# Optimization experiments

Hardware: AMD Instinct MI355X
Metric: run time of the kernel (lower is better)

The kernel has to match this reference:

```python
import jax, jax.numpy as jnp
import numpy as np

EMBED_DIM = 768
NUM_HEADS = 12
D_K = EMBED_DIM // NUM_HEADS


def setup_inputs() -> dict:
    key = jax.random.key(0)
    ks = jax.random.split(key, 9)
    b, s, d = 4, 2048, EMBED_DIM
    scale = 1.0 / np.sqrt(d)
    x = jax.random.normal(ks[0], (b, s, d), dtype=jnp.float32)
    return {
        "x": x,
        "w_q": jax.random.normal(ks[1], (d, d), dtype=jnp.float32) * scale,
        "b_q": jnp.zeros((d,), dtype=jnp.float32),
        "w_k": jax.random.normal(ks[2], (d, d), dtype=jnp.float32) * scale,
        "b_k": jnp.zeros((d,), dtype=jnp.float32),
        "w_v": jax.random.normal(ks[3], (d, d), dtype=jnp.float32) * scale,
        "b_v": jnp.zeros((d,), dtype=jnp.float32),
        "w_o": jax.random.normal(ks[4], (d, d), dtype=jnp.float32) * scale,
        "b_o": jnp.zeros((d,), dtype=jnp.float32),
    }


def reference(x, w_q, b_q, w_k, b_k, w_v, b_v, w_o, b_o):
    b, s, d = x.shape
    h, dk = NUM_HEADS, D_K
    # projections (torch Linear: x @ W^T + b)
    q = (x @ w_q.T + b_q).reshape(b, s, h, dk).transpose(0, 2, 1, 3)
    k = (x @ w_k.T + b_k).reshape(b, s, h, dk).transpose(0, 2, 1, 3)
    v = (x @ w_v.T + b_v).reshape(b, s, h, dk).transpose(0, 2, 1, 3)
    # causal attention: full [b,h,s,s] scores as in the original
    scores = jnp.einsum("bhqd,bhkd->bhqk", q, k) / jnp.sqrt(jnp.float32(dk))
    causal = jnp.tril(jnp.ones((s, s), dtype=bool))
    scores = jnp.where(causal[None, None], scores, -jnp.inf)
    attn = jax.nn.softmax(scores, axis=-1)
    out = jnp.einsum("bhqk,bhkd->bhqd", attn, v)
    out = out.transpose(0, 2, 1, 3).reshape(b, s, h * dk)
    return out @ w_o.T + b_o
```

## Files before the change

kernel.cpp:

```cpp
#include <hip/hip_runtime.h>
#include <hip/hip_bf16.h>
#include <stdint.h>

typedef short bf16x8 __attribute__((ext_vector_type(8)));
typedef float f32x4 __attribute__((ext_vector_type(4)));
typedef unsigned short u16;


__device__ __forceinline__ u16 f2bf_bits(float f) {
    __hip_bfloat16 h = __float2bfloat16(f);
    return __builtin_bit_cast(u16, h);
}

__device__ __forceinline__ uint32_t pack2bf(float a, float b) {
    uint32_t ua = __builtin_bit_cast(uint32_t, a) + 0x8000u;
    uint32_t ub = __builtin_bit_cast(uint32_t, b) + 0x8000u;
    return __builtin_amdgcn_perm(ub, ua, 0x07060302u);
}

__device__ __forceinline__ void gld_lds16(const void* g, void* l) {
    __builtin_amdgcn_global_load_lds(
        (const __attribute__((address_space(1))) void*)g,
        (__attribute__((address_space(3))) void*)l, 16, 0, 0);
}

#define CEXP 0.18033688011112042f


__global__ __launch_bounds__(256) void cast_all_kernel(
    const float* __restrict__ x, const float* __restrict__ w0,
    const float* __restrict__ w1, const float* __restrict__ w2,
    const float* __restrict__ w3, u16* __restrict__ xb,
    u16* __restrict__ o0, u16* __restrict__ o1,
    u16* __restrict__ o2, u16* __restrict__ o3,
    const float* __restrict__ bq, const float* __restrict__ bk,
    const float* __restrict__ bv, float* __restrict__ biasf) {
    int gid = blockIdx.x * 256 + threadIdx.x;
    const float* s;
    u16* d;
    int off;
    if (gid < 1572864) {
        s = x; d = xb; off = gid;
    } else {
        int g2 = gid - 1572864;
        int which = g2 / 147456;
        off = g2 - which * 147456;
        s = which == 0 ? w0 : which == 1 ? w1 : which == 2 ? w2 : w3;
        d = which == 0 ? o0 : which == 1 ? o1 : which == 2 ? o2 : o3;
    }
    float4 v = ((const float4*)s)[off];
    ushort4 u;
    u.x = f2bf_bits(v.x); u.y = f2bf_bits(v.y);
    u.z = f2bf_bits(v.z); u.w = f2bf_bits(v.w);
    ((ushort4*)d)[off] = u;
    if (gid < 2304) {
        float bb = gid < 768 ? bq[gid] : gid < 1536 ? bk[gid - 768] : bv[gid - 1536];
        biasf[gid] = bb;
    }
}


template <int RT, int MODE>
__global__ __launch_bounds__(256) void gemm_xwt(
    const u16* __restrict__ X, const u16* __restrict__ W,
    const float* __restrict__ bias, float* __restrict__ Cf,
    u16* __restrict__ Cb, u16* __restrict__ Vt, int K, int NC) {
    constexpr int JR = RT / 32;
    __shared__ u16 lsX[RT * 64];
    __shared__ u16 lsW[128 * 64];
    const int tid = threadIdx.x;
    const int w = tid >> 6, lane = tid & 63;
    const int quad = lane >> 4, l15 = lane & 15;
    const int m0 = blockIdx.y * RT, n0 = blockIdx.x * 128;
    const int wr = (w >> 1) * (RT / 2), wc = (w & 1) * 64;
    const int rr = lane >> 3, c8 = lane & 7;

    f32x4 acc[JR][4];
    for (int j = 0; j < JR; ++j)
        for (int i = 0; i < 4; ++i) acc[j][i] = (f32x4){0.f, 0.f, 0.f, 0.f};

    const int KT = K / 64;
    for (int kt = 0; kt < KT; ++kt) {
        const int k0 = kt * 64;
        __syncthreads();
        for (int cb = w; cb < RT / 8; cb += 4) {
            int row = cb * 8 + rr;
            int cg = c8 ^ ((rr ^ cb) & 7);
            gld_lds16(X + (size_t)(m0 + row) * K + k0 + cg * 8, &lsX[cb * 512]);
        }
        for (int cb = w; cb < 16; cb += 4) {
            int row = cb * 8 + rr;
            int cg = c8 ^ ((rr ^ cb) & 7);
            gld_lds16(W + (size_t)(n0 + row) * K + k0 + cg * 8, &lsW[cb * 512]);
        }
        __syncthreads();

        for (int kk = 0; kk < 2; ++kk) {
            bf16x8 xf[JR], wf[4];
            for (int j = 0; j < JR; ++j) {
                int row = wr + j * 16 + l15;
                int slot = (kk * 4 + quad) ^ ((row ^ (row >> 3)) & 7);
                xf[j] = *(const bf16x8*)&lsX[row * 64 + slot * 8];
            }
            for (int i = 0; i < 4; ++i) {
                int row = wc + i * 16 + l15;
                int slot = (kk * 4 + quad) ^ ((row ^ (row >> 3)) & 7);
                wf[i] = *(const bf16x8*)&lsW[row * 64 + slot * 8];
            }
            for (int j = 0; j < JR; ++j)
                for (int i = 0; i < 4; ++i)
                    acc[j][i] = __builtin_amdgcn_mfma_f32_16x16x32_bf16(
                        wf[i], xf[j], acc[j][i], 0, 0, 0);
        }
    }

    const bool vtile = (MODE == 2) && (n0 >= 1536);
    for (int i = 0; i < 4; ++i) {
        int c0 = n0 + wc + i * 16 + quad * 4;
        float4 bv4 = *(const float4*)&bias[c0];
        for (int j = 0; j < JR; ++j) {
            int row = m0 + wr + j * 16 + l15;
            float v0 = acc[j][i][0] + bv4.x;
            float v1 = acc[j][i][1] + bv4.y;
            float v2 = acc[j][i][2] + bv4.z;
            float v3 = acc[j][i][3] + bv4.w;
            if (MODE == 1) {
                float4 o4 = {v0, v1, v2, v3};
                *(float4*)&Cf[(size_t)row * NC + c0] = o4;
            } else if (vtile) {
                int d = c0 - 1536;
                int bq_ = row >> 11;
                int s = row & 2047;
                int h = d >> 6, dd = d & 63;
                size_t base = ((size_t)(bq_ * 12 + h) * 64 + dd) * 2048 + s;
                Vt[base]          = f2bf_bits(v0);
                Vt[base + 2048]   = f2bf_bits(v1);
                Vt[base + 4096]   = f2bf_bits(v2);
                Vt[base + 6144]   = f2bf_bits(v3);
            } else {
                uint2 pk = {pack2bf(v0, v1), pack2bf(v2, v3)};
                *(uint2*)&Cb[(size_t)row * NC + c0] = pk;
            }
        }
    }
}


__global__ __launch_bounds__(256, 3) void attn_kernel(
    const u16* __restrict__ QKV, const u16* __restrict__ Vt, u16* __restrict__ O) {
    __shared__ u16 lsQ[128 * 64];
    __shared__ u16 lsK[64 * 64];
    __shared__ u16 lsV[64 * 64];
    __shared__ u16 lsP[4][32 * 72];

    int bx = blockIdx.x;
    int bh = bx % 48;
    int qtb = 15 - (bx / 48);
    int b = bh / 12, h = bh % 12;
    int tid = threadIdx.x, w = tid >> 6, lane = tid & 63;
    int quad = lane >> 4, l15 = lane & 15;
    int rr = lane >> 3, c8 = lane & 7;

    for (int cb = w; cb < 16; cb += 4) {
        int row = cb * 8 + rr;
        int cg = c8 ^ ((rr ^ cb) & 7);
        gld_lds16(QKV + (size_t)(b * 2048 + qtb * 128 + row) * 2304 + h * 64 + cg * 8,
                  &lsQ[cb * 512]);
    }
    __syncthreads();

    bf16x8 q0[2], q1[2];
    for (int g = 0; g < 2; ++g) {
        int rowq = g * 64 + w * 16 + l15;
        int swq = (rowq ^ (rowq >> 3)) & 7;
        q0[g] = *(const bf16x8*)&lsQ[rowq * 64 + ((0 + quad) ^ swq) * 8];
        q1[g] = *(const bf16x8*)&lsQ[rowq * 64 + ((4 + quad) ^ swq) * 8];
    }

    f32x4 oacc0[4], oacc1[4];
    for (int dt = 0; dt < 4; ++dt) {
        oacc0[dt] = (f32x4){0.f, 0.f, 0.f, 0.f};
        oacc1[dt] = (f32x4){0.f, 0.f, 0.f, 0.f};
    }
    float li0 = 0.f, li1 = 0.f;
    u16* Pw = lsP[w];
    const int qrel = w * 16 + l15;
    const int ktmax = 2 * qtb + 1;

    for (int kt = 0; kt <= ktmax; ++kt) {
        __syncthreads();
        for (int cb = w; cb < 8; cb += 4) {
            int row = cb * 8 + rr;
            int cg = c8 ^ ((rr ^ cb) & 7);
            gld_lds16(QKV + (size_t)(b * 2048 + kt * 64 + row) * 2304 + 768 + h * 64 + cg * 8,
                      &lsK[cb * 512]);
            gld_lds16(Vt + (size_t)(bh * 64 + row) * 2048 + kt * 64 + cg * 8,
                      &lsV[cb * 512]);
        }
        __syncthreads();

        const bool do0 = (kt <= 2 * qtb);

        f32x4 S0[4], S1[4];
        for (int ct = 0; ct < 4; ++ct) {
            int rowk = ct * 16 + l15;
            int swk = (rowk ^ (rowk >> 3)) & 7;
            bf16x8 k0 = *(const bf16x8*)&lsK[rowk * 64 + ((0 + quad) ^ swk) * 8];
            bf16x8 k1 = *(const bf16x8*)&lsK[rowk * 64 + ((4 + quad) ^ swk) * 8];
            f32x4 z = (f32x4){0.f, 0.f, 0.f, 0.f};
            S1[ct] = __builtin_amdgcn_mfma_f32_16x16x32_bf16(k0, q0[1], z, 0, 0, 0);
            S1[ct] = __builtin_amdgcn_mfma_f32_16x16x32_bf16(k1, q1[1], S1[ct], 0, 0, 0);
            if (do0) {
                S0[ct] = __builtin_amdgcn_mfma_f32_16x16x32_bf16(k0, q0[0], z, 0, 0, 0);
                S0[ct] = __builtin_amdgcn_mfma_f32_16x16x32_bf16(k1, q1[0], S0[ct], 0, 0, 0);
            }
        }

        if (kt == 2 * qtb) {
            for (int ct = 0; ct < 4; ++ct) {
                int kbase = ct * 16 + quad * 4;
                for (int r = 0; r < 4; ++r)
                    if (kbase + r > qrel) S0[ct][r] = -1e30f;
            }
        }
        if (kt == 2 * qtb + 1) {
            for (int ct = 0; ct < 4; ++ct) {
                int kbase = ct * 16 + quad * 4;
                for (int r = 0; r < 4; ++r)
                    if (kbase + r > qrel) S1[ct][r] = -1e30f;
            }
        }

        if (do0) {
            u16* Pr = &Pw[(size_t)l15 * 72];
            for (int ct = 0; ct < 4; ++ct) {
                float p0 = __builtin_amdgcn_exp2f(S0[ct][0] * CEXP);
                float p1 = __builtin_amdgcn_exp2f(S0[ct][1] * CEXP);
                float p2 = __builtin_amdgcn_exp2f(S0[ct][2] * CEXP);
                float p3 = __builtin_amdgcn_exp2f(S0[ct][3] * CEXP);
                li0 += (p0 + p1) + (p2 + p3);
                uint2 pk = {pack2bf(p0, p1), pack2bf(p2, p3)};
                *(uint2*)&Pr[ct * 16 + quad * 4] = pk;
            }
        }
        {
            u16* Pr = &Pw[(size_t)(16 + l15) * 72];
            for (int ct = 0; ct < 4; ++ct) {
                float p0 = __builtin_amdgcn_exp2f(S1[ct][0] * CEXP);
                float p1 = __builtin_amdgcn_exp2f(S1[ct][1] * CEXP);
                float p2 = __builtin_amdgcn_exp2f(S1[ct][2] * CEXP);
                float p3 = __builtin_amdgcn_exp2f(S1[ct][3] * CEXP);
                li1 += (p0 + p1) + (p2 + p3);
                uint2 pk = {pack2bf(p0, p1), pack2bf(p2, p3)};
                *(uint2*)&Pr[ct * 16 + quad * 4] = pk;
            }
        }

        for (int ks = 0; ks < 2; ++ks) {
            bf16x8 bp1 = *(const bf16x8*)&Pw[(size_t)(16 + l15) * 72 + ks * 32 + quad * 8];
            bf16x8 bp0;
            if (do0) bp0 = *(const bf16x8*)&Pw[(size_t)l15 * 72 + ks * 32 + quad * 8];
            for (int dt = 0; dt < 4; ++dt) {
                int rowv = dt * 16 + l15;
                int swv = (rowv ^ (rowv >> 3)) & 7;
                bf16x8 av = *(const bf16x8*)&lsV[rowv * 64 + ((ks * 4 + quad) ^ swv) * 8];
                oacc1[dt] = __builtin_amdgcn_mfma_f32_16x16x32_bf16(av, bp1, oacc1[dt], 0, 0, 0);
                if (do0)
                    oacc0[dt] = __builtin_amdgcn_mfma_f32_16x16x32_bf16(av, bp0, oacc0[dt], 0, 0, 0);
            }
        }
    }

    li0 += __shfl_xor(li0, 16, 64);
    li0 += __shfl_xor(li0, 32, 64);
    li1 += __shfl_xor(li1, 16, 64);
    li1 += __shfl_xor(li1, 32, 64);
    float inv0 = 1.0f / li0, inv1 = 1.0f / li1;

    for (int g = 0; g < 2; ++g) {
        float inv = g ? inv1 : inv0;
        f32x4* oa = g ? oacc1 : oacc0;
        int row = qtb * 128 + g * 64 + w * 16 + l15;
        for (int dt = 0; dt < 4; ++dt) {
            uint2 pk = {pack2bf(oa[dt][0] * inv, oa[dt][1] * inv),
                        pack2bf(oa[dt][2] * inv, oa[dt][3] * inv)};
            *(uint2*)&O[(size_t)(b * 2048 + row) * 768 + h * 64 + dt * 16 + quad * 4] = pk;
        }
    }
}


extern "C" void kernel_launch(void* const* d_in, const int* in_sizes, int n_in,
                              void* d_out, int out_size, void* d_ws, size_t ws_size,
                              hipStream_t stream) {
    const float* x  = (const float*)d_in[0];
    const float* wq = (const float*)d_in[1];
    const float* bq = (const float*)d_in[2];
    const float* wk = (const float*)d_in[3];
    const float* bk = (const float*)d_in[4];
    const float* wv = (const float*)d_in[5];
    const float* bv = (const float*)d_in[6];
    const float* wo = (const float*)d_in[7];
    const float* bo = (const float*)d_in[8];
    float* out = (float*)d_out;

    char* ws = (char*)d_ws;
    u16*   xb    = (u16*)(ws + 0);
    u16*   Wf    = (u16*)(ws + 12582912);
    u16*   wob   = (u16*)(ws + 16121856);
    float* biasf = (float*)(ws + 17301504);
    u16*   QKVb  = (u16*)(ws + 17310720);
    u16*   Vtw   = (u16*)(ws + 55059456);
    u16*   Ow    = (u16*)(ws + 67642368);

    cast_all_kernel<<<8448, 256, 0, stream>>>(x, wq, wk, wv, wo,
                                              xb, Wf, Wf + 589824, Wf + 1179648, wob,
                                              bq, bk, bv, biasf);

    gemm_xwt<128, 2><<<dim3(18, 64), 256, 0, stream>>>(xb, Wf, biasf, nullptr, QKVb,
                                                       Vtw, 768, 2304);
    attn_kernel<<<768, 256, 0, stream>>>(QKVb, Vtw, Ow);
    gemm_xwt<64, 1><<<dim3(6, 128), 256, 0, stream>>>(Ow, wob, bo, out, nullptr,
                                                      nullptr, 768, 768);
}
```

Measured before the change: 215.3 us.

## Double-buffer GEMM and attention loads, fold softmax scale into Wq, MFMA row sums

The GEMM and attention kernels now double-buffer their LDS tiles, prefetching the next K tile while the current one is computed, so each iteration needs one barrier instead of two. The softmax exponent scale is folded into W_q and b_q during the cast, removing a multiply per score. Row sums are computed with an MFMA against a ones vector, replacing per-lane adds and cross-lane shuffles. The V-transpose epilogue is staged through LDS so it can use coalesced 16-byte stores, and launch-bound occupancy hints are added. The extra LDS may reduce occupancy, and summing the bf16-rounded probabilities slightly changes numerics.

```diff
diff --git a/kernel.cpp b/kernel.cpp
--- a/kernel.cpp
+++ b/kernel.cpp
@@ -39,6 +39,7 @@
     const float* s;
     u16* d;
     int off;
+    float mul = 1.0f;
     if (gid < 1572864) {
         s = x; d = xb; off = gid;
     } else {
@@ -47,27 +48,30 @@
         off = g2 - which * 147456;
         s = which == 0 ? w0 : which == 1 ? w1 : which == 2 ? w2 : w3;
         d = which == 0 ? o0 : which == 1 ? o1 : which == 2 ? o2 : o3;
+        if (which == 0) mul = CEXP;
     }
     float4 v = ((const float4*)s)[off];
     ushort4 u;
-    u.x = f2bf_bits(v.x); u.y = f2bf_bits(v.y);
-    u.z = f2bf_bits(v.z); u.w = f2bf_bits(v.w);
+    u.x = f2bf_bits(v.x * mul); u.y = f2bf_bits(v.y * mul);
+    u.z = f2bf_bits(v.z * mul); u.w = f2bf_bits(v.w * mul);
     ((ushort4*)d)[off] = u;
     if (gid < 2304) {
-        float bb = gid < 768 ? bq[gid] : gid < 1536 ? bk[gid - 768] : bv[gid - 1536];
+        float bb = gid < 768 ? bq[gid] * CEXP
+                             : gid < 1536 ? bk[gid - 768] : bv[gid - 1536];
         biasf[gid] = bb;
     }
 }
 
 
-template <int RT, int MODE>
-__global__ __launch_bounds__(256) void gemm_xwt(
+template <int RT, int MODE, int MINW>
+__global__ __launch_bounds__(256, MINW) void gemm_xwt(
     const u16* __restrict__ X, const u16* __restrict__ W,
     const float* __restrict__ bias, float* __restrict__ Cf,
     u16* __restrict__ Cb, u16* __restrict__ Vt, int K, int NC) {
     constexpr int JR = RT / 32;
-    __shared__ u16 lsX[RT * 64];
-    __shared__ u16 lsW[128 * 64];
+    constexpr int XSZ = RT * 64;
+    constexpr int WSZ = 128 * 64;
+    __shared__ u16 pool[2 * XSZ + 2 * WSZ];
     const int tid = threadIdx.x;
     const int w = tid >> 6, lane = tid & 63;
     const int quad = lane >> 4, l15 = lane & 15;
@@ -75,71 +79,97 @@
     const int wr = (w >> 1) * (RT / 2), wc = (w & 1) * 64;
     const int rr = lane >> 3, c8 = lane & 7;
 
+    auto stage = [&](int kt, int pb) {
+        const int k0 = kt * 64;
+        u16* bx = pool + pb * XSZ;
+        u16* bw = pool + 2 * XSZ + pb * WSZ;
+        for (int cb = w; cb < RT / 8; cb += 4) {
+            int row = cb * 8 + rr;
+            int cg = c8 ^ ((rr ^ cb) & 7);
+            gld_lds16(X + (size_t)(m0 + row) * K + k0 + cg * 8, &bx[cb * 512]);
+        }
+        for (int cb = w; cb < 16; cb += 4) {
+            int row = cb * 8 + rr;
+            int cg = c8 ^ ((rr ^ cb) & 7);
+            gld_lds16(W + (size_t)(n0 + row) * K + k0 + cg * 8, &bw[cb * 512]);
+        }
+    };
+
     f32x4 acc[JR][4];
     for (int j = 0; j < JR; ++j)
         for (int i = 0; i < 4; ++i) acc[j][i] = (f32x4){0.f, 0.f, 0.f, 0.f};
 
     const int KT = K / 64;
+    stage(0, 0);
+    __syncthreads();
     for (int kt = 0; kt < KT; ++kt) {
-        const int k0 = kt * 64;
-        __syncthreads();
-        for (int cb = w; cb < RT / 8; cb += 4) {
-            int row = cb * 8 + rr;
-            int cg = c8 ^ ((rr ^ cb) & 7);
-            gld_lds16(X + (size_t)(m0 + row) * K + k0 + cg * 8, &lsX[cb * 512]);
-        }
-        for (int cb = w; cb < 16; cb += 4) {
-            int row = cb * 8 + rr;
-            int cg = c8 ^ ((rr ^ cb) & 7);
-            gld_lds16(W + (size_t)(n0 + row) * K + k0 + cg * 8, &lsW[cb * 512]);
-        }
-        __syncthreads();
-
+        const int pb = kt & 1;
+        if (kt + 1 < KT) stage(kt + 1, pb ^ 1);
+        const u16* bx = pool + pb * XSZ;
+        const u16* bw = pool + 2 * XSZ + pb * WSZ;
         for (int kk = 0; kk < 2; ++kk) {
             bf16x8 xf[JR], wf[4];
             for (int j = 0; j < JR; ++j) {
                 int row = wr + j * 16 + l15;
                 int slot = (kk * 4 + quad) ^ ((row ^ (row >> 3)) & 7);
-                xf[j] = *(const bf16x8*)&lsX[row * 64 + slot * 8];
+                xf[j] = *(const bf16x8*)&bx[row * 64 + slot * 8];
             }
             for (int i = 0; i < 4; ++i) {
                 int row = wc + i * 16 + l15;
                 int slot = (kk * 4 + quad) ^ ((row ^ (row >> 3)) & 7);
-                wf[i] = *(const bf16x8*)&lsW[row * 64 + slot * 8];
+                wf[i] = *(const bf16x8*)&bw[row * 64 + slot * 8];
             }
             for (int j = 0; j < JR; ++j)
                 for (int i = 0; i < 4; ++i)
                     acc[j][i] = __builtin_amdgcn_mfma_f32_16x16x32_bf16(
                         wf[i], xf[j], acc[j][i], 0, 0, 0);
         }
+        __syncthreads();
     }
 
     const bool vtile = (MODE == 2) && (n0 >= 1536);
-    for (int i = 0; i < 4; ++i) {
-        int c0 = n0 + wc + i * 16 + quad * 4;
-        float4 bv4 = *(const float4*)&bias[c0];
-        for (int j = 0; j < JR; ++j) {
-            int row = m0 + wr + j * 16 + l15;
-            float v0 = acc[j][i][0] + bv4.x;
-            float v1 = acc[j][i][1] + bv4.y;
-            float v2 = acc[j][i][2] + bv4.z;
-            float v3 = acc[j][i][3] + bv4.w;
-            if (MODE == 1) {
-                float4 o4 = {v0, v1, v2, v3};
-                *(float4*)&Cf[(size_t)row * NC + c0] = o4;
-            } else if (vtile) {
-                int d = c0 - 1536;
-                int bq_ = row >> 11;
-                int s = row & 2047;
-                int h = d >> 6, dd = d & 63;
-                size_t base = ((size_t)(bq_ * 12 + h) * 64 + dd) * 2048 + s;
-                Vt[base]          = f2bf_bits(v0);
-                Vt[base + 2048]   = f2bf_bits(v1);
-                Vt[base + 4096]   = f2bf_bits(v2);
-                Vt[base + 6144]   = f2bf_bits(v3);
-            } else {
-                uint2 pk = {pack2bf(v0, v1), pack2bf(v2, v3)};
-                *(uint2*)&Cb[(size_t)row * NC + c0] = pk;
+    if (vtile) {
+        u16* T2 = pool;
+        for (int i = 0; i < 4; ++i) {
+            int nl = wc + i * 16 + quad * 4;
+            int c0 = n0 + nl;
+            float4 bv4 = *(const float4*)&bias[c0];
+            for (int j = 0; j < JR; ++j) {
+                int ml = wr + j * 16 + l15;
+                T2[(nl + 0) * 136 + ml] = f2bf_bits(acc[j][i][0] + bv4.x);
+                T2[(nl + 1) * 136 + ml] = f2bf_bits(acc[j][i][1] + bv4.y);
+                T2[(nl + 2) * 136 + ml] = f2bf_bits(acc[j][i][2] + bv4.z);
+                T2[(nl + 3) * 136 + ml] = f2bf_bits(acc[j][i][3] + bv4.w);
+            }
+        }
+        __syncthreads();
+        int sc = (tid & 15) * 8;
+        int bq_ = m0 >> 11;
+        int s0 = m0 & 2047;
+        for (int rnd = 0; rnd < 8; ++rnd) {
+            int dl = (tid >> 4) + rnd * 16;
+            bf16x8 vv = *(const bf16x8*)&T2[dl * 136 + sc];
+            int dg = n0 + dl - 1536;
+            int h = dg >> 6, dd = dg & 63;
+            *(bf16x8*)&Vt[((size_t)(bq_ * 12 + h) * 64 + dd) * 2048 + s0 + sc] = vv;
+        }
+    } else {
+        for (int i = 0; i < 4; ++i) {
+            int c0 = n0 + wc + i * 16 + quad * 4;
+            float4 bv4 = *(const float4*)&bias[c0];
+            for (int j = 0; j < JR; ++j) {
+                int row = m0 + wr + j * 16 + l15;
+                float v0 = acc[j][i][0] + bv4.x;
+                float v1 = acc[j][i][1] + bv4.y;
+                float v2 = acc[j][i][2] + bv4.z;
+                float v3 = acc[j][i][3] + bv4.w;
+                if (MODE == 1) {
+                    float4 o4 = {v0, v1, v2, v3};
+                    *(float4*)&Cf[(size_t)row * NC + c0] = o4;
+                } else {
+                    uint2 pk = {pack2bf(v0, v1), pack2bf(v2, v3)};
+                    *(uint2*)&Cb[(size_t)row * NC + c0] = pk;
+                }
             }
         }
     }
@@ -148,9 +178,7 @@
 
 __global__ __launch_bounds__(256, 3) void attn_kernel(
     const u16* __restrict__ QKV, const u16* __restrict__ Vt, u16* __restrict__ O) {
-    __shared__ u16 lsQ[128 * 64];
-    __shared__ u16 lsK[64 * 64];
-    __shared__ u16 lsV[64 * 64];
+    __shared__ u16 lsKV[2 * 128 * 64];
     __shared__ u16 lsP[4][32 * 72];
 
     int bx = blockIdx.x;
@@ -161,52 +189,66 @@
     int quad = lane >> 4, l15 = lane & 15;
     int rr = lane >> 3, c8 = lane & 7;
 
-    for (int cb = w; cb < 16; cb += 4) {
-        int row = cb * 8 + rr;
-        int cg = c8 ^ ((rr ^ cb) & 7);
-        gld_lds16(QKV + (size_t)(b * 2048 + qtb * 128 + row) * 2304 + h * 64 + cg * 8,
-                  &lsQ[cb * 512]);
-    }
+    auto stageKV = [&](int kt, int pb) {
+        u16* dst = lsKV + pb * 8192;
+        for (int cb = w; cb < 16; cb += 4) {
+            int r = (cb & 7) * 8 + rr;
+            int cg = c8 ^ ((rr ^ cb) & 7);
+            const u16* g = (cb < 8)
+                ? QKV + (size_t)(b * 2048 + kt * 64 + r) * 2304 + 768 + h * 64 + cg * 8
+                : Vt + (size_t)(bh * 64 + r) * 2048 + kt * 64 + cg * 8;
+            gld_lds16(g, &dst[cb * 512]);
+        }
+    };
+
+    {
+        u16* qs = lsKV + 8192;
+        for (int cb = w; cb < 16; cb += 4) {
+            int row = cb * 8 + rr;
+            int cg = c8 ^ ((rr ^ cb) & 7);
+            gld_lds16(QKV + (size_t)(b * 2048 + qtb * 128 + row) * 2304 + h * 64 + cg * 8,
+                      &qs[cb * 512]);
+        }
+    }
+    stageKV(0, 0);
     __syncthreads();
 
     bf16x8 q0[2], q1[2];
     for (int g = 0; g < 2; ++g) {
+        const u16* qs = lsKV + 8192;
         int rowq = g * 64 + w * 16 + l15;
         int swq = (rowq ^ (rowq >> 3)) & 7;
-        q0[g] = *(const bf16x8*)&lsQ[rowq * 64 + ((0 + quad) ^ swq) * 8];
-        q1[g] = *(const bf16x8*)&lsQ[rowq * 64 + ((4 + quad) ^ swq) * 8];
-    }
-
-    f32x4 oacc0[4], oacc1[4];
+        q0[g] = *(const bf16x8*)&qs[rowq * 64 + ((0 + quad) ^ swq) * 8];
+        q1[g] = *(const bf16x8*)&qs[rowq * 64 + ((4 + quad) ^ swq) * 8];
+    }
+    __syncthreads();
+
+    const bf16x8 ones = {(short)0x3F80, (short)0x3F80, (short)0x3F80, (short)0x3F80,
+                         (short)0x3F80, (short)0x3F80, (short)0x3F80, (short)0x3F80};
+    f32x4 oacc0[4], oacc1[4], lacc0, lacc1;
     for (int dt = 0; dt < 4; ++dt) {
         oacc0[dt] = (f32x4){0.f, 0.f, 0.f, 0.f};
         oacc1[dt] = (f32x4){0.f, 0.f, 0.f, 0.f};
     }
-    float li0 = 0.f, li1 = 0.f;
+    lacc0 = (f32x4){0.f, 0.f, 0.f, 0.f};
+    lacc1 = (f32x4){0.f, 0.f, 0.f, 0.f};
     u16* Pw = lsP[w];
     const int qrel = w * 16 + l15;
     const int ktmax = 2 * qtb + 1;
 
     for (int kt = 0; kt <= ktmax; ++kt) {
-        __syncthreads();
-        for (int cb = w; cb < 8; cb += 4) {
-            int row = cb * 8 + rr;
-            int cg = c8 ^ ((rr ^ cb) & 7);
-            gld_lds16(QKV + (size_t)(b * 2048 + kt * 64 + row) * 2304 + 768 + h * 64 + cg * 8,
-                      &lsK[cb * 512]);
-            gld_lds16(Vt + (size_t)(bh * 64 + row) * 2048 + kt * 64 + cg * 8,
-                      &lsV[cb * 512]);
-        }
-        __syncthreads();
-
+        const int pb = kt & 1;
+        if (kt < ktmax) stageKV(kt + 1, pb ^ 1);
+        const u16* Kf = lsKV + pb * 8192;
+        const u16* Vf = Kf + 4096;
         const bool do0 = (kt <= 2 * qtb);
 
         f32x4 S0[4], S1[4];
         for (int ct = 0; ct < 4; ++ct) {
             int rowk = ct * 16 + l15;
             int swk = (rowk ^ (rowk >> 3)) & 7;
-            bf16x8 k0 = *(const bf16x8*)&lsK[rowk * 64 + ((0 + quad) ^ swk) * 8];
-            bf16x8 k1 = *(const bf16x8*)&lsK[rowk * 64 + ((4 + quad) ^ swk) * 8];
+            bf16x8 k0 = *(const bf16x8*)&Kf[rowk * 64 + ((0 + quad) ^ swk) * 8];
+            bf16x8 k1 = *(const bf16x8*)&Kf[rowk * 64 + ((4 + quad) ^ swk) * 8];
             f32x4 z = (f32x4){0.f, 0.f, 0.f, 0.f};
             S1[ct] = __builtin_amdgcn_mfma_f32_16x16x32_bf16(k0, q0[1], z, 0, 0, 0);
             S1[ct] = __builtin_amdgcn_mfma_f32_16x16x32_bf16(k1, q1[1], S1[ct], 0, 0, 0);
@@ -234,11 +276,10 @@
         if (do0) {
             u16* Pr = &Pw[(size_t)l15 * 72];
             for (int ct = 0; ct < 4; ++ct) {
-                float p0 = __builtin_amdgcn_exp2f(S0[ct][0] * CEXP);
-                float p1 = __builtin_amdgcn_exp2f(S0[ct][1] * CEXP);
-                float p2 = __builtin_amdgcn_exp2f(S0[ct][2] * CEXP);
-                float p3 = __builtin_amdgcn_exp2f(S0[ct][3] * CEXP);
-                li0 += (p0 + p1) + (p2 + p3);
+                float p0 = __builtin_amdgcn_exp2f(S0[ct][0]);
+                float p1 = __builtin_amdgcn_exp2f(S0[ct][1]);
+                float p2 = __builtin_amdgcn_exp2f(S0[ct][2]);
+                float p3 = __builtin_amdgcn_exp2f(S0[ct][3]);
                 uint2 pk = {pack2bf(p0, p1), pack2bf(p2, p3)};
                 *(uint2*)&Pr[ct * 16 + quad * 4] = pk;
             }
@@ -246,11 +287,10 @@
         {
             u16* Pr = &Pw[(size_t)(16 + l15) * 72];
             for (int ct = 0; ct < 4; ++ct) {
-                float p0 = __builtin_amdgcn_exp2f(S1[ct][0] * CEXP);
-                float p1 = __builtin_amdgcn_exp2f(S1[ct][1] * CEXP);
-                float p2 = __builtin_amdgcn_exp2f(S1[ct][2] * CEXP);
-                float p3 = __builtin_amdgcn_exp2f(S1[ct][3] * CEXP);
-                li1 += (p0 + p1) + (p2 + p3);
+                float p0 = __builtin_amdgcn_exp2f(S1[ct][0]);
+                float p1 = __builtin_amdgcn_exp2f(S1[ct][1]);
+                float p2 = __builtin_amdgcn_exp2f(S1[ct][2]);
+                float p3 = __builtin_amdgcn_exp2f(S1[ct][3]);
                 uint2 pk = {pack2bf(p0, p1), pack2bf(p2, p3)};
                 *(uint2*)&Pr[ct * 16 + quad * 4] = pk;
             }
@@ -260,23 +300,22 @@
             bf16x8 bp1 = *(const bf16x8*)&Pw[(size_t)(16 + l15) * 72 + ks * 32 + quad * 8];
             bf16x8 bp0;
             if (do0) bp0 = *(const bf16x8*)&Pw[(size_t)l15 * 72 + ks * 32 + quad * 8];
+            lacc1 = __builtin_amdgcn_mfma_f32_16x16x32_bf16(ones, bp1, lacc1, 0, 0, 0);
+            if (do0)
+                lacc0 = __builtin_amdgcn_mfma_f32_16x16x32_bf16(ones, bp0, lacc0, 0, 0, 0);
             for (int dt = 0; dt < 4; ++dt) {
                 int rowv = dt * 16 + l15;
                 int swv = (rowv ^ (rowv >> 3)) & 7;
-                bf16x8 av = *(const bf16x8*)&lsV[rowv * 64 + ((ks * 4 + quad) ^ swv) * 8];
+                bf16x8 av = *(const bf16x8*)&Vf[rowv * 64 + ((ks * 4 + quad) ^ swv) * 8];
                 oacc1[dt] = __builtin_amdgcn_mfma_f32_16x16x32_bf16(av, bp1, oacc1[dt], 0, 0, 0);
                 if (do0)
                     oacc0[dt] = __builtin_amdgcn_mfma_f32_16x16x32_bf16(av, bp0, oacc0[dt], 0, 0, 0);
             }
         }
-    }
-
-    li0 += __shfl_xor(li0, 16, 64);
-    li0 += __shfl_xor(li0, 32, 64);
-    li1 += __shfl_xor(li1, 16, 64);
-    li1 += __shfl_xor(li1, 32, 64);
-    float inv0 = 1.0f / li0, inv1 = 1.0f / li1;
-
+        __syncthreads();
+    }
+
+    float inv0 = 1.0f / lacc0[0], inv1 = 1.0f / lacc1[0];
     for (int g = 0; g < 2; ++g) {
         float inv = g ? inv1 : inv0;
         f32x4* oa = g ? oacc1 : oacc0;
@@ -317,9 +356,9 @@
                                               xb, Wf, Wf + 589824, Wf + 1179648, wob,
                                               bq, bk, bv, biasf);
 
-    gemm_xwt<128, 2><<<dim3(18, 64), 256, 0, stream>>>(xb, Wf, biasf, nullptr, QKVb,
-                                                       Vtw, 768, 2304);
+    gemm_xwt<128, 2, 2><<<dim3(18, 64), 256, 0, stream>>>(xb, Wf, biasf, nullptr,
+                                                          QKVb, Vtw, 768, 2304);
     attn_kernel<<<768, 256, 0, stream>>>(QKVb, Vtw, Ow);
-    gemm_xwt<64, 1><<<dim3(6, 128), 256, 0, stream>>>(Ow, wob, bo, out, nullptr,
-                                                      nullptr, 768, 768);
-}
+    gemm_xwt<64, 1, 3><<<dim3(6, 128), 256, 0, stream>>>(Ow, wob, bo, out, nullptr,
+                                                         nullptr, 768, 768);
+}
```

New measurement: 221.1 us. 1.03x slower.
